# Optimization experiments

Hardware: AMD Instinct MI355X
Metric: run time of the kernel (lower is better)

## Reference

```python
import jax, jax.numpy as jnp
import numpy as np

N_NODES = 10000
N_EDGES = 160000
HIDDEN = 256
HEADS = 8
LN_EPS = 1e-5


def setup_inputs() -> dict:
    key = jax.random.key(0)
    ks = jax.random.split(key, 8)
    s = 1.0 / np.sqrt(HIDDEN)
    return {
        "node_embeddings": jax.random.normal(ks[0], (1, N_NODES, HIDDEN), jnp.float32),
        "edge_index": jax.random.randint(ks[1], (2, N_EDGES), 0, N_NODES, dtype=jnp.int32),
        "Wq": jax.random.normal(ks[2], (HIDDEN, HIDDEN), jnp.float32) * s,
        "Wk": jax.random.normal(ks[3], (HIDDEN, HIDDEN), jnp.float32) * s,
        "Wv": jax.random.normal(ks[4], (HIDDEN, HIDDEN), jnp.float32) * s,
        "Wo": jax.random.normal(ks[5], (HIDDEN, HIDDEN), jnp.float32) * s,
        "ln_gamma": jnp.ones((HIDDEN,), jnp.float32),
        "ln_beta": jnp.zeros((HIDDEN,), jnp.float32),
    }


def reference(node_embeddings, edge_index, Wq, Wk, Wv, Wo, ln_gamma, ln_beta):
    B, N, Dm = node_embeddings.shape
    H = HEADS
    hd = Dm // H
    scale = 1.0 / np.sqrt(hd)

    def heads(x):  # [B,N,Dm] -> [B,H,N,hd]
        return x.reshape(B, N, H, hd).transpose(0, 2, 1, 3)

    Q = heads(node_embeddings @ Wq)
    K = heads(node_embeddings @ Wk)
    V = heads(node_embeddings @ Wv)

    src, dst = edge_index[0], edge_index[1]
    Qe = Q[:, :, src, :]           # [B,H,E,hd]
    Ke = K[:, :, dst, :]
    Ve = V[:, :, dst, :]

    scores = jnp.einsum('bhed,bhed->bhe', Qe, Ke) * scale   # [B,H,E]
    s_t = scores.transpose(2, 0, 1)                          # [E,B,H]
    smax = jax.ops.segment_max(s_t, src, num_segments=N)    # [N,B,H]
    ex = jnp.exp(s_t - smax[src])                            # [E,B,H]
    denom = jax.ops.segment_sum(ex, src, num_segments=N)    # [N,B,H]
    attn = ex / denom[src]                                   # scatter-softmax weights

    wV = attn[..., None] * Ve.transpose(2, 0, 1, 3)          # [E,B,H,hd]
    agg = jax.ops.segment_sum(wV, src, num_segments=N)      # [N,B,H,hd]
    attn_out = agg.transpose(1, 0, 2, 3).reshape(B, N, Dm)   # [B,N,Dm]

    out = attn_out @ Wo
    x = out + node_embeddings
    mu = jnp.mean(x, axis=-1, keepdims=True)
    var = jnp.mean((x - mu) ** 2, axis=-1, keepdims=True)
    return (x - mu) * jax.lax.rsqrt(var + LN_EPS) * ln_gamma + ln_beta
```

## Files before the change

### kernel.cpp

```cpp
#include <hip/hip_runtime.h>

#define NN 10000
#define NE 160000
#define DM 256
#define CAP 96
#define LN_EPSF 1e-5f
#define SCALEF 0.17677669529663687f

typedef unsigned short u16;
typedef __attribute__((ext_vector_type(4))) u16 u16x4;
typedef __attribute__((ext_vector_type(8))) u16 u16x8;
typedef __attribute__((ext_vector_type(4))) float f32x4;
typedef __attribute__((ext_vector_type(8))) short short8;

__device__ __forceinline__ float b2f(u16 u) { return __uint_as_float(((unsigned)u) << 16); }
__device__ __forceinline__ u16 f2b(float f) {
    unsigned u = __float_as_uint(f);
    return (u16)((u + 0x7fffu + ((u >> 16) & 1u)) >> 16);
}
__device__ __forceinline__ int clampi(int v) { return v < 0 ? 0 : (v >= NN ? NN - 1 : v); }

__global__ void k_fill_zero_f32(float* __restrict__ o, int n) {
    int i = blockIdx.x * 256 + threadIdx.x;
    if (i < n) o[i] = 0.f;
}

__global__ void k_prep(const float* __restrict__ Wq, const float* __restrict__ Wk,
                       const float* __restrict__ Wv, const float* __restrict__ Wo,
                       u16* __restrict__ Wt, int* __restrict__ cnt) {
    int id = blockIdx.x * 256 + threadIdx.x;
    if (id < NN) cnt[id] = 0;
    int m = id >> 16;
    int rc = id & 65535;
    int r = rc >> 8, c = rc & 255;
    const float* W = (m == 0) ? Wq : (m == 1) ? Wk : (m == 2) ? Wv : Wo;
    Wt[m * 65536 + c * 256 + r] = f2b(W[r * 256 + c]);
}

__global__ void k_bucket(const int* __restrict__ ei, int* __restrict__ cnt, int* __restrict__ buck) {
    int e = blockIdx.x * 256 + threadIdx.x;
    if (e < NE) {
        int s = clampi(ei[e]);
        int slot = atomicAdd(&cnt[s], 1);
        if (slot < CAP) buck[s * CAP + slot] = clampi(ei[NE + e]);
    }
}

__global__ __launch_bounds__(256) void k_gemm_qkv(const float* __restrict__ X, const u16* __restrict__ Wt,
                                                  u16* __restrict__ Q, u16* __restrict__ KV) {
    constexpr int AS = 40;
    __shared__ u16 At[64 * AS];
    __shared__ u16 Bt[256 * AS];
    const int t = threadIdx.x;
    const int w = t >> 6, l = t & 63, quad = l >> 4, m16 = l & 15;
    const int mat = blockIdx.y;
    const u16* Wm = Wt + mat * 65536;
    const int node0 = blockIdx.x * 64;
    f32x4 acc[16];
#pragma unroll
    for (int i = 0; i < 16; i++) acc[i] = (f32x4){0.f, 0.f, 0.f, 0.f};
    const int arow = t >> 2, ac8 = (t & 3) * 8;
    for (int k0 = 0; k0 < DM; k0 += 32) {
        u16x8 av = {0, 0, 0, 0, 0, 0, 0, 0};
        int anode = node0 + arow;
        if (anode < NN) {
            const float* xp = X + (size_t)anode * DM + k0 + ac8;
            f32x4 a0 = *(const f32x4*)(xp);
            f32x4 a1 = *(const f32x4*)(xp + 4);
            av[0] = f2b(a0[0]); av[1] = f2b(a0[1]); av[2] = f2b(a0[2]); av[3] = f2b(a0[3]);
            av[4] = f2b(a1[0]); av[5] = f2b(a1[1]); av[6] = f2b(a1[2]); av[7] = f2b(a1[3]);
        }
        *(u16x8*)(At + arow * AS + ac8) = av;
        const u16* bsrc = Wm + t * DM + k0;
        u16x8 b0 = *(const u16x8*)(bsrc);
        u16x8 b1 = *(const u16x8*)(bsrc + 8);
        u16x8 b2 = *(const u16x8*)(bsrc + 16);
        u16x8 b3 = *(const u16x8*)(bsrc + 24);
        u16* bd = Bt + t * AS;
        *(u16x8*)(bd) = b0;
        *(u16x8*)(bd + 8) = b1;
        *(u16x8*)(bd + 16) = b2;
        *(u16x8*)(bd + 24) = b3;
        __syncthreads();
        short8 a = *(const short8*)(At + (w * 16 + m16) * AS + quad * 8);
#pragma unroll
        for (int ct = 0; ct < 16; ct++) {
            short8 b = *(const short8*)(Bt + (ct * 16 + m16) * AS + quad * 8);
            acc[ct] = __builtin_amdgcn_mfma_f32_16x16x32_bf16(a, b, acc[ct], 0, 0, 0);
        }
        __syncthreads();
    }
#pragma unroll
    for (int ct = 0; ct < 16; ct++) {
        int col = ct * 16 + m16;
#pragma unroll
        for (int r = 0; r < 4; r++) {
            int node = node0 + w * 16 + quad * 4 + r;
            if (node < NN) {
                u16 v = f2b(acc[ct][r]);
                if (mat == 0) Q[(size_t)node * DM + col] = v;
                else KV[(size_t)node * 512 + (col >> 2) * 8 + (col & 3) + ((mat == 2) ? 4 : 0)] = v;
            }
        }
    }
}

__global__ __launch_bounds__(256) void k_edge(const u16* __restrict__ Q, const u16* __restrict__ KV,
                                              const int* __restrict__ cnt, const int* __restrict__ buck,
                                              u16* __restrict__ attn) {
    const int t = threadIdx.x;
    const int w = t >> 6, l = t & 63;
    const int node = blockIdx.x * 4 + w;
    const int d0 = l * 4;
    int deg = cnt[node];
    if (deg > CAP) deg = CAP;
    const int* bl = buck + node * CAP;
    u16x4 q4 = *(const u16x4*)(Q + (size_t)node * DM + d0);
    float qf0 = b2f(q4[0]) * SCALEF, qf1 = b2f(q4[1]) * SCALEF;
    float qf2 = b2f(q4[2]) * SCALEF, qf3 = b2f(q4[3]) * SCALEF;
    float m = -3.0e38f, s = 0.f;
    float a0 = 0.f, a1 = 0.f, a2 = 0.f, a3 = 0.f;
    for (int i = 0; i < deg; i++) {
        int dst = bl[i];
        u16x8 kv = *(const u16x8*)(KV + (size_t)dst * 512 + l * 8);
        float p = qf0 * b2f(kv[0]) + qf1 * b2f(kv[1]) + qf2 * b2f(kv[2]) + qf3 * b2f(kv[3]);
        p += __shfl_xor(p, 1, 64);
        p += __shfl_xor(p, 2, 64);
        p += __shfl_xor(p, 4, 64);
        float nm = fmaxf(m, p);
        float al = __expf(m - nm);
        float pe = __expf(p - nm);
        s = s * al + pe;
        a0 = a0 * al + pe * b2f(kv[4]);
        a1 = a1 * al + pe * b2f(kv[5]);
        a2 = a2 * al + pe * b2f(kv[6]);
        a3 = a3 * al + pe * b2f(kv[7]);
        m = nm;
    }
    float inv = (s > 0.f) ? 1.f / s : 0.f;
    u16x4 o;
    o[0] = f2b(a0 * inv);
    o[1] = f2b(a1 * inv);
    o[2] = f2b(a2 * inv);
    o[3] = f2b(a3 * inv);
    *(u16x4*)(attn + (size_t)node * DM + d0) = o;
}

__global__ __launch_bounds__(256) void k_gemm_out_ln(const u16* __restrict__ In, const u16* __restrict__ WoT,
                                                     const float* __restrict__ X, const float* __restrict__ g,
                                                     const float* __restrict__ b, float* __restrict__ out) {
    constexpr int AS = 40;
    __shared__ u16 At[64 * AS];
    __shared__ u16 Bt[256 * AS];
    __shared__ float gl[256], bl[256];
    const int t = threadIdx.x;
    gl[t] = g[t];
    bl[t] = b[t];
    const int w = t >> 6, l = t & 63, quad = l >> 4, m16 = l & 15;
    const int node0 = blockIdx.x * 64;
    f32x4 acc[16];
#pragma unroll
    for (int i = 0; i < 16; i++) acc[i] = (f32x4){0.f, 0.f, 0.f, 0.f};
    const int arow = t >> 2, ac8 = (t & 3) * 8;
    for (int k0 = 0; k0 < DM; k0 += 32) {
        u16x8 av = {0, 0, 0, 0, 0, 0, 0, 0};
        int anode = node0 + arow;
        if (anode < NN) av = *(const u16x8*)(In + (size_t)anode * DM + k0 + ac8);
        *(u16x8*)(At + arow * AS + ac8) = av;
        const u16* bsrc = WoT + t * DM + k0;
        u16x8 b0 = *(const u16x8*)(bsrc);
        u16x8 b1 = *(const u16x8*)(bsrc + 8);
        u16x8 b2 = *(const u16x8*)(bsrc + 16);
        u16x8 b3 = *(const u16x8*)(bsrc + 24);
        u16* bd = Bt + t * AS;
        *(u16x8*)(bd) = b0;
        *(u16x8*)(bd + 8) = b1;
        *(u16x8*)(bd + 16) = b2;
        *(u16x8*)(bd + 24) = b3;
        __syncthreads();
        short8 a = *(const short8*)(At + (w * 16 + m16) * AS + quad * 8);
#pragma unroll
        for (int ct = 0; ct < 16; ct++) {
            short8 bfr = *(const short8*)(Bt + (ct * 16 + m16) * AS + quad * 8);
            acc[ct] = __builtin_amdgcn_mfma_f32_16x16x32_bf16(a, bfr, acc[ct], 0, 0, 0);
        }
        __syncthreads();
    }
    float val[16][4];
    const int nodeBase = node0 + w * 16 + quad * 4;
#pragma unroll
    for (int ct = 0; ct < 16; ct++) {
        int col = ct * 16 + m16;
#pragma unroll
        for (int r = 0; r < 4; r++) {
            int node = nodeBase + r;
            float x = (node < NN) ? X[(size_t)node * DM + col] : 0.f;
            val[ct][r] = acc[ct][r] + x;
        }
    }
    float mu[4], rstd[4];
#pragma unroll
    for (int r = 0; r < 4; r++) {
        float s1 = 0.f, s2 = 0.f;
#pragma unroll
        for (int ct = 0; ct < 16; ct++) {
            float v = val[ct][r];
            s1 += v;
            s2 += v * v;
        }
#pragma unroll
        for (int o = 1; o < 16; o <<= 1) {
            s1 += __shfl_xor(s1, o, 64);
            s2 += __shfl_xor(s2, o, 64);
        }
        float mm = s1 * (1.f / DM);
        float var = s2 * (1.f / DM) - mm * mm;
        mu[r] = mm;
        rstd[r] = rsqrtf(var + LN_EPSF);
    }
#pragma unroll
    for (int ct = 0; ct < 16; ct++) {
        int col = ct * 16 + m16;
#pragma unroll
        for (int r = 0; r < 4; r++) {
            int node = nodeBase + r;
            if (node < NN)
                out[(size_t)node * DM + col] = (val[ct][r] - mu[r]) * rstd[r] * gl[col] + bl[col];
        }
    }
}

extern "C" void kernel_launch(void* const* d_in, const int* in_sizes, int n_in,
                              void* d_out, int out_size, void* d_ws, size_t ws_size,
                              hipStream_t stream) {
    (void)in_sizes; (void)n_in;
    const float* X  = (const float*)d_in[0];
    const int*   EI = (const int*)d_in[1];
    const float* Wq = (const float*)d_in[2];
    const float* Wk = (const float*)d_in[3];
    const float* Wv = (const float*)d_in[4];
    const float* Wo = (const float*)d_in[5];
    const float* g  = (const float*)d_in[6];
    const float* be = (const float*)d_in[7];

    const size_t SWT  = (size_t)4 * 65536 * 2;
    const size_t SKV  = (size_t)NN * 512 * 2;
    const size_t SAT  = (size_t)NN * DM * 2;
    const size_t SCNT = (size_t)NN * 4;
    const size_t SBK  = (size_t)NN * CAP * 4;
    const size_t need = SWT + SKV + SAT + SCNT + SBK;
    if (ws_size < need) {
        k_fill_zero_f32<<<(out_size + 255) / 256, 256, 0, stream>>>((float*)d_out, out_size);
        return;
    }
    char* p = (char*)d_ws;
    u16* Wt   = (u16*)p; p += SWT;
    u16* KVb  = (u16*)p; p += SKV;
    u16* attn = (u16*)p; p += SAT;
    int* cnt  = (int*)p; p += SCNT;
    int* buck = (int*)p; p += SBK;
    u16* Qb = (u16*)d_out;

    k_prep<<<1024, 256, 0, stream>>>(Wq, Wk, Wv, Wo, Wt, cnt);
    k_bucket<<<(NE + 255) / 256, 256, 0, stream>>>(EI, cnt, buck);
    k_gemm_qkv<<<dim3(157, 3), 256, 0, stream>>>(X, Wt, Qb, KVb);
    k_edge<<<NN / 4, 256, 0, stream>>>(Qb, KVb, cnt, buck, attn);
    k_gemm_out_ln<<<157, 256, 0, stream>>>(attn, Wt + 3 * 65536, X, g, be, (float*)d_out);
}
```

Measured before the change: 158.6 us.

## Merge edge bucketing into QKV GEMM launch and drop LDS staging in GEMMs

Edge bucketing and the QKV projection now run in one launch: blockIdx.y==3 does bucketing, and the first 157 blocks of the other rows do the GEMM. This removes one kernel launch and lets the two independent workloads overlap. Both GEMMs now load A and B fragments straight from global memory (weights stay L2-resident) instead of staging them through shared memory, which removes the barriers and LDS traffic. The cost is redundant global loads of the weight tiles by every wave, and many idle blocks in the padded grid.

```diff
diff --git a/kernel.cpp b/kernel.cpp
--- a/kernel.cpp
+++ b/kernel.cpp
@@ -37,58 +37,46 @@
     Wt[m * 65536 + c * 256 + r] = f2b(W[r * 256 + c]);
 }
 
-__global__ void k_bucket(const int* __restrict__ ei, int* __restrict__ cnt, int* __restrict__ buck) {
-    int e = blockIdx.x * 256 + threadIdx.x;
-    if (e < NE) {
-        int s = clampi(ei[e]);
-        int slot = atomicAdd(&cnt[s], 1);
-        if (slot < CAP) buck[s * CAP + slot] = clampi(ei[NE + e]);
-    }
-}
-
-__global__ __launch_bounds__(256) void k_gemm_qkv(const float* __restrict__ X, const u16* __restrict__ Wt,
-                                                  u16* __restrict__ Q, u16* __restrict__ KV) {
-    constexpr int AS = 40;
-    __shared__ u16 At[64 * AS];
-    __shared__ u16 Bt[256 * AS];
+__global__ __launch_bounds__(256) void k_qkv_bucket(const float* __restrict__ X, const u16* __restrict__ Wt,
+                                                    u16* __restrict__ Q, u16* __restrict__ KV,
+                                                    const int* __restrict__ EI, int* __restrict__ cnt,
+                                                    int* __restrict__ buck) {
+    if (blockIdx.y == 3) {
+        int e = blockIdx.x * 256 + threadIdx.x;
+        if (e < NE) {
+            int s = clampi(EI[e]);
+            int slot = atomicAdd(&cnt[s], 1);
+            if (slot < CAP) buck[s * CAP + slot] = clampi(EI[NE + e]);
+        }
+        return;
+    }
+    if (blockIdx.x >= 157) return;
     const int t = threadIdx.x;
     const int w = t >> 6, l = t & 63, quad = l >> 4, m16 = l & 15;
     const int mat = blockIdx.y;
     const u16* Wm = Wt + mat * 65536;
     const int node0 = blockIdx.x * 64;
+    const int arow = node0 + w * 16 + m16;
     f32x4 acc[16];
 #pragma unroll
     for (int i = 0; i < 16; i++) acc[i] = (f32x4){0.f, 0.f, 0.f, 0.f};
-    const int arow = t >> 2, ac8 = (t & 3) * 8;
+#pragma unroll
     for (int k0 = 0; k0 < DM; k0 += 32) {
-        u16x8 av = {0, 0, 0, 0, 0, 0, 0, 0};
-        int anode = node0 + arow;
-        if (anode < NN) {
-            const float* xp = X + (size_t)anode * DM + k0 + ac8;
+        short8 a = {0, 0, 0, 0, 0, 0, 0, 0};
+        if (arow < NN) {
+            const float* xp = X + (size_t)arow * DM + k0 + quad * 8;
             f32x4 a0 = *(const f32x4*)(xp);
             f32x4 a1 = *(const f32x4*)(xp + 4);
-            av[0] = f2b(a0[0]); av[1] = f2b(a0[1]); av[2] = f2b(a0[2]); av[3] = f2b(a0[3]);
-            av[4] = f2b(a1[0]); av[5] = f2b(a1[1]); av[6] = f2b(a1[2]); av[7] = f2b(a1[3]);
-        }
-        *(u16x8*)(At + arow * AS + ac8) = av;
-        const u16* bsrc = Wm + t * DM + k0;
-        u16x8 b0 = *(const u16x8*)(bsrc);
-        u16x8 b1 = *(const u16x8*)(bsrc + 8);
-        u16x8 b2 = *(const u16x8*)(bsrc + 16);
-        u16x8 b3 = *(const u16x8*)(bsrc + 24);
-        u16* bd = Bt + t * AS;
-        *(u16x8*)(bd) = b0;
-        *(u16x8*)(bd + 8) = b1;
-        *(u16x8*)(bd + 16) = b2;
-        *(u16x8*)(bd + 24) = b3;
-        __syncthreads();
-        short8 a = *(const short8*)(At + (w * 16 + m16) * AS + quad * 8);
+            a[0] = (short)f2b(a0[0]); a[1] = (short)f2b(a0[1]);
+            a[2] = (short)f2b(a0[2]); a[3] = (short)f2b(a0[3]);
+            a[4] = (short)f2b(a1[0]); a[5] = (short)f2b(a1[1]);
+            a[6] = (short)f2b(a1[2]); a[7] = (short)f2b(a1[3]);
+        }
 #pragma unroll
         for (int ct = 0; ct < 16; ct++) {
-            short8 b = *(const short8*)(Bt + (ct * 16 + m16) * AS + quad * 8);
+            short8 b = *(const short8*)(Wm + (ct * 16 + m16) * DM + k0 + quad * 8);
             acc[ct] = __builtin_amdgcn_mfma_f32_16x16x32_bf16(a, b, acc[ct], 0, 0, 0);
         }
-        __syncthreads();
     }
 #pragma unroll
     for (int ct = 0; ct < 16; ct++) {
@@ -149,42 +137,26 @@
 __global__ __launch_bounds__(256) void k_gemm_out_ln(const u16* __restrict__ In, const u16* __restrict__ WoT,
                                                      const float* __restrict__ X, const float* __restrict__ g,
                                                      const float* __restrict__ b, float* __restrict__ out) {
-    constexpr int AS = 40;
-    __shared__ u16 At[64 * AS];
-    __shared__ u16 Bt[256 * AS];
     __shared__ float gl[256], bl[256];
     const int t = threadIdx.x;
     gl[t] = g[t];
     bl[t] = b[t];
+    __syncthreads();
     const int w = t >> 6, l = t & 63, quad = l >> 4, m16 = l & 15;
     const int node0 = blockIdx.x * 64;
+    const int arow = node0 + w * 16 + m16;
     f32x4 acc[16];
 #pragma unroll
     for (int i = 0; i < 16; i++) acc[i] = (f32x4){0.f, 0.f, 0.f, 0.f};
-    const int arow = t >> 2, ac8 = (t & 3) * 8;
+#pragma unroll
     for (int k0 = 0; k0 < DM; k0 += 32) {
-        u16x8 av = {0, 0, 0, 0, 0, 0, 0, 0};
-        int anode = node0 + arow;
-        if (anode < NN) av = *(const u16x8*)(In + (size_t)anode * DM + k0 + ac8);
-        *(u16x8*)(At + arow * AS + ac8) = av;
-        const u16* bsrc = WoT + t * DM + k0;
-        u16x8 b0 = *(const u16x8*)(bsrc);
-        u16x8 b1 = *(const u16x8*)(bsrc + 8);
-        u16x8 b2 = *(const u16x8*)(bsrc + 16);
-        u16x8 b3 = *(const u16x8*)(bsrc + 24);
-        u16* bd = Bt + t * AS;
-        *(u16x8*)(bd) = b0;
-        *(u16x8*)(bd + 8) = b1;
-        *(u16x8*)(bd + 16) = b2;
-        *(u16x8*)(bd + 24) = b3;
-        __syncthreads();
-        short8 a = *(const short8*)(At + (w * 16 + m16) * AS + quad * 8);
+        short8 a = {0, 0, 0, 0, 0, 0, 0, 0};
+        if (arow < NN) a = *(const short8*)(In + (size_t)arow * DM + k0 + quad * 8);
 #pragma unroll
         for (int ct = 0; ct < 16; ct++) {
-            short8 bfr = *(const short8*)(Bt + (ct * 16 + m16) * AS + quad * 8);
+            short8 bfr = *(const short8*)(WoT + (ct * 16 + m16) * DM + k0 + quad * 8);
             acc[ct] = __builtin_amdgcn_mfma_f32_16x16x32_bf16(a, bfr, acc[ct], 0, 0, 0);
         }
-        __syncthreads();
     }
     float val[16][4];
     const int nodeBase = node0 + w * 16 + quad * 4;
@@ -262,8 +234,7 @@
     u16* Qb = (u16*)d_out;
 
     k_prep<<<1024, 256, 0, stream>>>(Wq, Wk, Wv, Wo, Wt, cnt);
-    k_bucket<<<(NE + 255) / 256, 256, 0, stream>>>(EI, cnt, buck);
-    k_gemm_qkv<<<dim3(157, 3), 256, 0, stream>>>(X, Wt, Qb, KVb);
+    k_qkv_bucket<<<dim3(625, 4), 256, 0, stream>>>(X, Wt, Qb, KVb, EI, cnt, buck);
     k_edge<<<NN / 4, 256, 0, stream>>>(Qb, KVb, cnt, buck, attn);
     k_gemm_out_ln<<<157, 256, 0, stream>>>(attn, Wt + 3 * 65536, X, g, be, (float*)d_out);
 }
```

After: 189.2 us. +19.3%, slower.
